# Performance work log

Measured on AMD Instinct MI355X. Metric: run time of the kernel, lower is better.

## Reference

```python
import jax, jax.numpy as jnp
import numpy as np

NUM_POINTS = 500_000
NUM_SUP = 8192
DEGREE = 32
HIDDEN = 256
NDIM = 3


def sincos_embed(coords, dim):
    # Faithful port of kappamodules ContinuousSincosEmbed.
    ndim = coords.shape[-1]
    ndim_padding = dim % ndim
    dim_per = (dim - ndim_padding) // ndim
    sincos_padding = dim_per % 2
    padding = ndim_padding + sincos_padding * ndim
    eff = (dim - padding) // ndim  # even
    omega = 1.0 / (10000.0 ** (jnp.arange(0, eff, 2, dtype=jnp.float32) / eff))
    out = coords[..., None] * omega  # (N, ndim, eff//2)
    emb = jnp.concatenate([jnp.sin(out), jnp.cos(out)], axis=-1)  # (N, ndim, eff)
    emb = emb.reshape(coords.shape[:-1] + (ndim * eff,))
    if padding > 0:
        emb = jnp.pad(emb, [(0, 0)] * (emb.ndim - 1) + [(0, padding)])
    return emb


def setup_inputs() -> dict:
    key = jax.random.key(0)
    ks = jax.random.split(key, 8)
    input_pos = jax.random.uniform(ks[0], (NUM_POINTS, NDIM), dtype=jnp.float32)
    supernode_idx = jnp.sort(
        jax.random.randint(ks[1], (NUM_SUP,), 0, NUM_POINTS, dtype=jnp.int32)
    )
    src_idx = jax.random.randint(ks[2], (NUM_SUP * DEGREE,), 0, NUM_POINTS, dtype=jnp.int32)
    dst_seg = jnp.repeat(jnp.arange(NUM_SUP, dtype=jnp.int32), DEGREE)
    s = 1.0 / np.sqrt(HIDDEN)
    w1 = jax.random.normal(ks[3], (HIDDEN, HIDDEN), dtype=jnp.float32) * s
    w2 = jax.random.normal(ks[4], (HIDDEN, HIDDEN), dtype=jnp.float32) * s
    wp = jax.random.normal(ks[5], (2 * HIDDEN, HIDDEN), dtype=jnp.float32) / np.sqrt(2 * HIDDEN)
    b1 = jnp.zeros((HIDDEN,), jnp.float32)
    b2 = jnp.zeros((HIDDEN,), jnp.float32)
    bp = jnp.zeros((HIDDEN,), jnp.float32)
    return {
        "input_pos": input_pos, "supernode_idx": supernode_idx,
        "src_idx": src_idx, "dst_seg": dst_seg,
        "w1": w1, "b1": b1, "w2": w2, "b2": b2, "wp": wp, "bp": bp,
    }


def reference(input_pos, supernode_idx, src_idx, dst_seg, w1, b1, w2, b2, wp, bp):
    num_sup = supernode_idx.shape[0]
    sup_pos = input_pos[supernode_idx]            # (S, 3)
    src_pos = input_pos[src_idx]                  # (E, 3)
    dst_pos = sup_pos[dst_seg]                    # (E, 3)
    dist = dst_pos - src_pos
    mag = jnp.linalg.norm(dist, axis=1, keepdims=True)
    rel = jnp.concatenate([dist, mag], axis=1)    # (E, 4)
    x = sincos_embed(rel, HIDDEN)                 # (E, H) relpos embed, ndim=4
    # message MLP: Linear -> GELU(exact) -> Linear
    x = jax.nn.gelu(x @ w1 + b1, approximate=False) @ w2 + b2
    # segment mean into supernodes (dst is sorted/consecutive per supernode)
    sums = jax.ops.segment_sum(x, dst_seg, num_segments=num_sup)
    counts = jax.ops.segment_sum(jnp.ones((x.shape[0],), x.dtype), dst_seg, num_segments=num_sup)
    agg = sums / jnp.maximum(counts, 1.0)[:, None]  # (S, H)
    sup_embed = sincos_embed(sup_pos, HIDDEN)       # (S, H) abspos embed, ndim=3
    out = jnp.concatenate([agg, sup_embed], axis=-1) @ wp + bp  # (S, H)
    return out[None]  # (1, S, H) -- batch_size=1 (batch_idx=None)
```

## Files before the change

### kernel.cpp

```cpp
#include <hip/hip_runtime.h>
#include <hip/hip_bf16.h>

typedef __bf16 bf16_t;
typedef bf16_t bf16x8 __attribute__((ext_vector_type(8)));
typedef float f32x16 __attribute__((ext_vector_type(16)));

constexpr float OMG[16] = {
    1.0f,        0.74989421f, 0.56234133f, 0.42169650f,
    0.31622777f, 0.23713737f, 0.17782794f, 0.13335214f,
    0.1f,        0.074989421f, 0.056234133f, 0.042169650f,
    0.031622777f, 0.023713737f, 0.017782794f, 0.013335214f};

__device__ __forceinline__ f32x16 mfma_bf16(bf16x8 a, bf16x8 b, f32x16 c) {
  return __builtin_amdgcn_mfma_f32_32x32x16_bf16(a, b, c, 0, 0, 0);
}

__device__ __forceinline__ int orig_k(int pk) {
  return 64 * (pk >> 5) + 32 * ((pk >> 4) & 1) + (pk & 15);
}

__global__ __launch_bounds__(256) void prep(
    const float* __restrict__ w1, const float* __restrict__ w2,
    const float* __restrict__ wp, const float* __restrict__ b1,
    const float* __restrict__ b2, const float* __restrict__ bp,
    bf16_t* __restrict__ w1img, bf16_t* __restrict__ wpT2,
    float* __restrict__ bfold, float* __restrict__ b1fold) {
  __shared__ float T[256][33];
  const int bid = blockIdx.x;
  const int tid = threadIdx.x;

  if (bid < 8) {
    const int n0 = bid * 32;
#pragma unroll
    for (int it = 0; it < 16; ++it) {
      const int pk = it * 8 + (tid >> 5);
      T[pk][tid & 31] = w1[orig_k(pk) * 256 + n0 + (tid & 31)];
    }
    __syncthreads();
    const int n_off = tid & 31;
    const int n = n0 + n_off;
#pragma unroll
    for (int q = 0; q < 2; ++q) {
      const int slot = (tid >> 5) + 8 * q;
      bf16x8 v;
#pragma unroll
      for (int e = 0; e < 8; ++e) v[e] = (bf16_t)T[slot * 8 + e][n_off];
      *(bf16x8*)((char*)w1img + n * 256 + ((slot ^ (n & 15)) << 4)) = v;
    }
  } else if (bid == 8) {
    const int n = tid;
    float vl[4];
    float bf1 = b1[n];
#pragma unroll
    for (int d = 0; d < 4; ++d) {
      float s = 0.f;
#pragma unroll
      for (int i = 0; i < 16; ++i)
        s = fmaf(0.01f * OMG[i], w1[(64 * d + 16 + i) * 256 + n], s);
      vl[d] = s;
#pragma unroll
      for (int i = 0; i < 16; ++i) bf1 += w1[(64 * d + 48 + i) * 256 + n];
    }
    bf16_t* ext = w1img + 32768 + n * 16;
#pragma unroll
    for (int e = 0; e < 4; ++e) ext[e] = (bf16_t)vl[e];
#pragma unroll
    for (int e = 4; e < 16; ++e) ext[e] = (bf16_t)0.0f;
    b1fold[n] = bf1;
  } else if (bid < 17) {
    const int band = (bid - 9) * 32;
#pragma unroll
    for (int it = 0; it < 32; ++it)
      T[tid][it] = wp[(256 + band + it) * 256 + tid];
    __syncthreads();
    const int o = tid;
#pragma unroll
    for (int g = 0; g < 4; ++g) {
      bf16x8 v;
#pragma unroll
      for (int e = 0; e < 8; ++e) v[e] = (bf16_t)T[o][g * 8 + e];
      *(bf16x8*)(wpT2 + o * 512 + 256 + band + g * 8) = v;
    }
  } else if (bid < 81) {
    const int t2 = bid - 17;
    const int o0 = (t2 >> 3) * 32, j0 = (t2 & 7) * 32;
#pragma unroll
    for (int it = 0; it < 32; ++it) {
      const int n = it * 8 + (tid >> 5);
      T[n][tid & 31] = wp[n * 256 + o0 + (tid & 31)];
    }
    __syncthreads();
    const int o_off = tid & 31, jb = tid >> 5;
    float a4[4] = {0.f, 0.f, 0.f, 0.f};
    for (int n = 0; n < 256; ++n) {
      const float wv = T[n][o_off];
#pragma unroll
      for (int q = 0; q < 4; ++q)
        a4[q] = fmaf(w2[(j0 + jb + 8 * q) * 256 + n], wv, a4[q]);
    }
#pragma unroll
    for (int q = 0; q < 4; ++q)
      wpT2[(o0 + o_off) * 512 + j0 + jb + 8 * q] = (bf16_t)a4[q];
  } else {
    const int o = (bid - 81) * 8 + (tid >> 5);
    const int kl = (tid & 31) * 8;
    float s = 0.f;
#pragma unroll
    for (int k = 0; k < 8; ++k) s += b2[kl + k] * wp[(kl + k) * 256 + o];
    s += __shfl_xor(s, 16); s += __shfl_xor(s, 8); s += __shfl_xor(s, 4);
    s += __shfl_xor(s, 2); s += __shfl_xor(s, 1);
    if ((tid & 31) == 0) bfold[o] = s + bp[o];
  }
}

__global__ __launch_bounds__(512, 4) void edge_mlp(
    const float* __restrict__ pos, const int* __restrict__ sup_idx,
    const int* __restrict__ src_idx,
    const bf16_t* __restrict__ w1img, const float* __restrict__ b1fold,
    bf16_t* __restrict__ cat) {
  __shared__ __attribute__((aligned(16))) bf16_t Bs[36864];

  const int tid = threadIdx.x;

  {
    const bf16x8* src8 = (const bf16x8*)w1img;
    bf16x8* dst8 = (bf16x8*)Bs;
#pragma unroll
    for (int it = 0; it < 9; ++it) {
      const int idx = it * 512 + tid;
      dst8[idx] = src8[idx];
    }
  }

  const int l = tid & 63, w = tid >> 6;
  const int pair = w >> 1, half = w & 1;
  const int hi = l >> 5, lc = l & 31;
  const int s = blockIdx.x * 4 + pair;

  const int si = sup_idx[s];
  const int srci = src_idx[s * 32 + lc];
  const float dx = pos[si * 3 + 0] - pos[srci * 3 + 0];
  const float dy = pos[si * 3 + 1] - pos[srci * 3 + 1];
  const float dz = pos[si * 3 + 2] - pos[srci * 3 + 2];
  const float mg = sqrtf(dx * dx + dy * dy + dz * dz);
  const float rv[4] = {dx, dy, dz, mg};

  float omg[8];
#pragma unroll
  for (int e = 0; e < 8; ++e) omg[e] = hi ? OMG[8 + e] : OMG[e];

  __syncthreads();

  f32x16 acc[4];
#pragma unroll
  for (int nt = 0; nt < 4; ++nt)
#pragma unroll
    for (int p = 0; p < 16; ++p) acc[nt][p] = 0.0f;

  const char* Bb = (const char*)Bs;
  const int sxor = (lc & 15) << 4;
  const int rowbase = (128 * half + lc) * 256;

  {
    bf16x8 aext;
#pragma unroll
    for (int e = 0; e < 8; ++e)
      aext[e] = (hi == 0 && e < 4) ? (bf16_t)rv[e] : (bf16_t)0.0f;
    const char* eb = Bb + 65536 + (128 * half + lc) * 32 + hi * 16;
#pragma unroll
    for (int nt = 0; nt < 4; ++nt) {
      bf16x8 be = *(const bf16x8*)(eb + nt * 1024);
      acc[nt] = mfma_bf16(aext, be, acc[nt]);
    }
  }

#pragma unroll
  for (int d = 0; d < 4; ++d) {
    float ang[8];
#pragma unroll
    for (int e = 0; e < 8; ++e) ang[e] = rv[d] * omg[e];
    bf16x8 a_sin, a_cos;
#pragma unroll
    for (int e = 0; e < 8; ++e) a_sin[e] = (bf16_t)__sinf(ang[e]);
#pragma unroll
    for (int e = 0; e < 8; ++e) a_cos[e] = (bf16_t)__cosf(ang[e]);

    const int ko_sin = ((4 * d + hi) << 4) ^ sxor;
    const int ko_cos = ((4 * d + 2 + hi) << 4) ^ sxor;
    {
      bf16x8 b0 = *(const bf16x8*)(Bb + rowbase + 0 * 8192 + ko_sin);
      bf16x8 b1_ = *(const bf16x8*)(Bb + rowbase + 1 * 8192 + ko_sin);
      bf16x8 b2_ = *(const bf16x8*)(Bb + rowbase + 2 * 8192 + ko_sin);
      bf16x8 b3 = *(const bf16x8*)(Bb + rowbase + 3 * 8192 + ko_sin);
      acc[0] = mfma_bf16(a_sin, b0, acc[0]);
      acc[1] = mfma_bf16(a_sin, b1_, acc[1]);
      acc[2] = mfma_bf16(a_sin, b2_, acc[2]);
      acc[3] = mfma_bf16(a_sin, b3, acc[3]);
    }
    {
      bf16x8 b0 = *(const bf16x8*)(Bb + rowbase + 0 * 8192 + ko_cos);
      bf16x8 b1_ = *(const bf16x8*)(Bb + rowbase + 1 * 8192 + ko_cos);
      bf16x8 b2_ = *(const bf16x8*)(Bb + rowbase + 2 * 8192 + ko_cos);
      bf16x8 b3 = *(const bf16x8*)(Bb + rowbase + 3 * 8192 + ko_cos);
      acc[0] = mfma_bf16(a_cos, b0, acc[0]);
      acc[1] = mfma_bf16(a_cos, b1_, acc[1]);
      acc[2] = mfma_bf16(a_cos, b2_, acc[2]);
      acc[3] = mfma_bf16(a_cos, b3, acc[3]);
    }
  }

  const float C2 = -0.10296644f, C0 = -2.3022765f;
#pragma unroll
  for (int nt = 0; nt < 4; ++nt) {
    const float bi = b1fold[128 * half + 32 * nt + lc];
    float ssum = 0.0f;
#pragma unroll
    for (int p = 0; p < 16; p += 2) {
      const float x0 = acc[nt][p] + bi;
      const float x1 = acc[nt][p + 1] + bi;
      const float t0 = fmaf(x0 * x0, C2, C0), t1 = fmaf(x1 * x1, C2, C0);
      const float e0 = exp2f(x0 * t0), e1 = exp2f(x1 * t1);
      const float r0 = __builtin_amdgcn_rcpf(e0 + 1.0f);
      const float r1 = __builtin_amdgcn_rcpf(e1 + 1.0f);
      ssum = fmaf(x0, r0, ssum);
      ssum = fmaf(x1, r1, ssum);
    }
    ssum += __shfl_xor(ssum, 32);
    if (hi == 0)
      cat[s * 512 + 128 * half + 32 * nt + lc] = (bf16_t)(ssum * 0.03125f);
  }

#pragma unroll
  for (int q = 0; q < 2; ++q) {
    const int col = 128 * half + l + 64 * q;
    float v = 0.0f;
    if (col < 252) {
      const int d = (col >= 84 ? 1 : 0) + (col >= 168 ? 1 : 0);
      const int t3 = col - 84 * d;
      const int sc2 = (t3 >= 42) ? 1 : 0;
      const float om = __expf(-0.21929381838038533f * (float)(t3 - 42 * sc2));
      const float pd = pos[si * 3 + d];
      const float ang = pd * om;
      v = sc2 ? __cosf(ang) : __sinf(ang);
    }
    cat[s * 512 + 256 + col] = (bf16_t)v;
  }
}

__global__ __launch_bounds__(256) void proj(
    const bf16_t* __restrict__ cat, const bf16_t* __restrict__ wpT2,
    const float* __restrict__ bfold, float* __restrict__ out) {
  const int tid = threadIdx.x;
  const int l = tid & 63, w = tid >> 6;
  const int hi = l >> 5, lc = l & 31;
  const int rm = blockIdx.x * 32;
  const int cn = blockIdx.y * 128 + w * 32;
  const int r0 = rm + lc;
  const int c0 = cn + lc;

  f32x16 a0;
#pragma unroll
  for (int p = 0; p < 16; ++p) a0[p] = 0.f;
#pragma unroll 8
  for (int kk = 0; kk < 32; ++kk) {
    int k0 = kk * 16 + 8 * hi;
    bf16x8 fa0 = *(const bf16x8*)(cat + r0 * 512 + k0);
    bf16x8 fb = *(const bf16x8*)(wpT2 + c0 * 512 + k0);
    a0 = mfma_bf16(fa0, fb, a0);
  }
  float bias = bfold[c0];
#pragma unroll
  for (int rr = 0; rr < 16; ++rr) {
    int rowo = (rr & 3) + 8 * (rr >> 2) + 4 * hi;
    out[(rm + rowo) * 256 + c0] = a0[rr] + bias;
  }
}

extern "C" void kernel_launch(void* const* d_in, const int* in_sizes, int n_in,
                              void* d_out, int out_size, void* d_ws, size_t ws_size,
                              hipStream_t stream) {
  const float* pos = (const float*)d_in[0];
  const int* sup_idx = (const int*)d_in[1];
  const int* src_idx = (const int*)d_in[2];
  const float* w1 = (const float*)d_in[4];
  const float* b1 = (const float*)d_in[5];
  const float* w2 = (const float*)d_in[6];
  const float* b2 = (const float*)d_in[7];
  const float* wp = (const float*)d_in[8];
  const float* bp = (const float*)d_in[9];

  char* ws = (char*)d_ws;
  bf16_t* w1img = (bf16_t*)(ws);
  bf16_t* wpT2  = (bf16_t*)(ws + 73728);
  float*  bfold = (float*)(ws + 335872);
  float*  b1fold = (float*)(ws + 336896);
  bf16_t* cat   = (bf16_t*)(ws + 337920);
  float* out = (float*)d_out;

  if (ws_size < (size_t)(337920 + 8192 * 512 * 2)) return;

  prep<<<dim3(113), dim3(256), 0, stream>>>(
      w1, w2, wp, b1, b2, bp, w1img, wpT2, bfold, b1fold);
  edge_mlp<<<dim3(2048), dim3(512), 0, stream>>>(pos, sup_idx, src_idx, w1img, b1fold, cat);
  proj<<<dim3(256, 2), dim3(256), 0, stream>>>(cat, wpT2, bfold, out);
}
```

Measured before the change: 78.27 us.

## Fold W2·Wp with MFMA, loop supernodes per block, and widen proj tiles

The scalar FMA fold of w2 into wp in the prep kernel is replaced by a bf16 conversion pass plus a separate small MFMA GEMM kernel. The edge MLP kernel now processes four supernodes per wave pair in a loop, so each block loads the shared-memory w1 image once for 16 supernodes instead of 4, and the grid shrinks fourfold. The projection kernel computes two 32-row tiles per wave, reusing each weight fragment across both. The costs are an extra kernel launch, a bf16-rounded folded weight, fewer blocks to fill the GPU, and a serial loop that may hurt latency hiding.

Result: slower. 143.9 us (+83.8%).

```diff
diff --git a/kernel.cpp b/kernel.cpp
--- a/kernel.cpp
+++ b/kernel.cpp
@@ -19,11 +19,12 @@
   return 64 * (pk >> 5) + 32 * ((pk >> 4) & 1) + (pk & 15);
 }
 
-__global__ __launch_bounds__(256) void prep(
+__global__ __launch_bounds__(256) void prepA(
     const float* __restrict__ w1, const float* __restrict__ w2,
     const float* __restrict__ wp, const float* __restrict__ b1,
     const float* __restrict__ b2, const float* __restrict__ bp,
     bf16_t* __restrict__ w1img, bf16_t* __restrict__ wpT2,
+    bf16_t* __restrict__ wpTa, bf16_t* __restrict__ w2b,
     float* __restrict__ bfold, float* __restrict__ b1fold) {
   __shared__ float T[256][33];
   const int bid = blockIdx.x;
@@ -81,28 +82,29 @@
       for (int e = 0; e < 8; ++e) v[e] = (bf16_t)T[o][g * 8 + e];
       *(bf16x8*)(wpT2 + o * 512 + 256 + band + g * 8) = v;
     }
-  } else if (bid < 81) {
-    const int t2 = bid - 17;
-    const int o0 = (t2 >> 3) * 32, j0 = (t2 & 7) * 32;
+  } else if (bid < 25) {
+    const int band = (bid - 17) * 32;
+#pragma unroll
+    for (int it = 0; it < 32; ++it)
+      T[tid][it] = wp[(band + it) * 256 + tid];
+    __syncthreads();
+    const int o = tid;
+#pragma unroll
+    for (int g = 0; g < 4; ++g) {
+      bf16x8 v;
+#pragma unroll
+      for (int e = 0; e < 8; ++e) v[e] = (bf16_t)T[o][g * 8 + e];
+      *(bf16x8*)(wpTa + o * 256 + band + g * 8) = v;
+    }
+  } else if (bid < 33) {
+    const int base = (bid - 25) * 8192;
 #pragma unroll
     for (int it = 0; it < 32; ++it) {
-      const int n = it * 8 + (tid >> 5);
-      T[n][tid & 31] = wp[n * 256 + o0 + (tid & 31)];
-    }
-    __syncthreads();
-    const int o_off = tid & 31, jb = tid >> 5;
-    float a4[4] = {0.f, 0.f, 0.f, 0.f};
-    for (int n = 0; n < 256; ++n) {
-      const float wv = T[n][o_off];
-#pragma unroll
-      for (int q = 0; q < 4; ++q)
-        a4[q] = fmaf(w2[(j0 + jb + 8 * q) * 256 + n], wv, a4[q]);
-    }
-#pragma unroll
-    for (int q = 0; q < 4; ++q)
-      wpT2[(o0 + o_off) * 512 + j0 + jb + 8 * q] = (bf16_t)a4[q];
+      const int idx = base + it * 256 + tid;
+      w2b[idx] = (bf16_t)w2[idx];
+    }
   } else {
-    const int o = (bid - 81) * 8 + (tid >> 5);
+    const int o = (bid - 33) * 8 + (tid >> 5);
     const int kl = (tid & 31) * 8;
     float s = 0.f;
 #pragma unroll
@@ -110,6 +112,45 @@
     s += __shfl_xor(s, 16); s += __shfl_xor(s, 8); s += __shfl_xor(s, 4);
     s += __shfl_xor(s, 2); s += __shfl_xor(s, 1);
     if ((tid & 31) == 0) bfold[o] = s + bp[o];
+  }
+}
+
+__global__ __launch_bounds__(256) void prep_b(
+    const bf16_t* __restrict__ wpTa, const bf16_t* __restrict__ w2b,
+    bf16_t* __restrict__ wpT2) {
+  const int tid = threadIdx.x;
+  const int l = tid & 63;
+  const int w = tid >> 6;
+  const int wm = w >> 1, wn = w & 1;
+  const int rm = blockIdx.x * 128 + wm * 64;
+  const int cn = blockIdx.y * 128 + wn * 64;
+  const int asel = l >> 5;
+  const int lr = l & 31;
+  const int r0 = rm + lr, r1 = rm + 32 + lr;
+  const int c0 = cn + lr, c1 = cn + 32 + lr;
+
+  f32x16 a00, a01, a10, a11;
+#pragma unroll
+  for (int q = 0; q < 16; ++q) { a00[q] = 0.f; a01[q] = 0.f; a10[q] = 0.f; a11[q] = 0.f; }
+#pragma unroll 4
+  for (int kk = 0; kk < 16; ++kk) {
+    int k0 = kk * 16 + 8 * asel;
+    bf16x8 fa0 = *(const bf16x8*)(wpTa + r0 * 256 + k0);
+    bf16x8 fa1 = *(const bf16x8*)(wpTa + r1 * 256 + k0);
+    bf16x8 fb0 = *(const bf16x8*)(w2b + c0 * 256 + k0);
+    bf16x8 fb1 = *(const bf16x8*)(w2b + c1 * 256 + k0);
+    a00 = mfma_bf16(fa0, fb0, a00);
+    a01 = mfma_bf16(fa0, fb1, a01);
+    a10 = mfma_bf16(fa1, fb0, a10);
+    a11 = mfma_bf16(fa1, fb1, a11);
+  }
+#pragma unroll
+  for (int rr = 0; rr < 16; ++rr) {
+    int rowo = (rr & 3) + 8 * (rr >> 2) + 4 * asel;
+    wpT2[(rm + rowo) * 512 + c0] = (bf16_t)a00[rr];
+    wpT2[(rm + rowo) * 512 + c1] = (bf16_t)a01[rr];
+    wpT2[(rm + 32 + rowo) * 512 + c0] = (bf16_t)a10[rr];
+    wpT2[(rm + 32 + rowo) * 512 + c1] = (bf16_t)a11[rr];
   }
 }
 
@@ -135,115 +176,118 @@
   const int l = tid & 63, w = tid >> 6;
   const int pair = w >> 1, half = w & 1;
   const int hi = l >> 5, lc = l & 31;
-  const int s = blockIdx.x * 4 + pair;
-
-  const int si = sup_idx[s];
-  const int srci = src_idx[s * 32 + lc];
-  const float dx = pos[si * 3 + 0] - pos[srci * 3 + 0];
-  const float dy = pos[si * 3 + 1] - pos[srci * 3 + 1];
-  const float dz = pos[si * 3 + 2] - pos[srci * 3 + 2];
-  const float mg = sqrtf(dx * dx + dy * dy + dz * dz);
-  const float rv[4] = {dx, dy, dz, mg};
 
   float omg[8];
 #pragma unroll
   for (int e = 0; e < 8; ++e) omg[e] = hi ? OMG[8 + e] : OMG[e];
 
   __syncthreads();
-
-  f32x16 acc[4];
-#pragma unroll
-  for (int nt = 0; nt < 4; ++nt)
-#pragma unroll
-    for (int p = 0; p < 16; ++p) acc[nt][p] = 0.0f;
 
   const char* Bb = (const char*)Bs;
   const int sxor = (lc & 15) << 4;
   const int rowbase = (128 * half + lc) * 256;
-
-  {
-    bf16x8 aext;
-#pragma unroll
-    for (int e = 0; e < 8; ++e)
-      aext[e] = (hi == 0 && e < 4) ? (bf16_t)rv[e] : (bf16_t)0.0f;
-    const char* eb = Bb + 65536 + (128 * half + lc) * 32 + hi * 16;
+  const char* eb = Bb + 65536 + (128 * half + lc) * 32 + hi * 16;
+
+#pragma unroll 1
+  for (int ss = 0; ss < 4; ++ss) {
+    const int s = blockIdx.x * 16 + pair * 4 + ss;
+    const int si = sup_idx[s];
+    const int srci = src_idx[s * 32 + lc];
+    const float dx = pos[si * 3 + 0] - pos[srci * 3 + 0];
+    const float dy = pos[si * 3 + 1] - pos[srci * 3 + 1];
+    const float dz = pos[si * 3 + 2] - pos[srci * 3 + 2];
+    const float mg = sqrtf(dx * dx + dy * dy + dz * dz);
+    const float rv[4] = {dx, dy, dz, mg};
+
+    f32x16 acc[4];
+#pragma unroll
+    for (int nt = 0; nt < 4; ++nt)
+#pragma unroll
+      for (int p = 0; p < 16; ++p) acc[nt][p] = 0.0f;
+
+    {
+      bf16x8 aext;
+#pragma unroll
+      for (int e = 0; e < 8; ++e)
+        aext[e] = (hi == 0 && e < 4) ? (bf16_t)rv[e] : (bf16_t)0.0f;
+#pragma unroll
+      for (int nt = 0; nt < 4; ++nt) {
+        bf16x8 be = *(const bf16x8*)(eb + nt * 1024);
+        acc[nt] = mfma_bf16(aext, be, acc[nt]);
+      }
+    }
+
+#pragma unroll
+    for (int d = 0; d < 4; ++d) {
+      float ang[8];
+#pragma unroll
+      for (int e = 0; e < 8; ++e) ang[e] = rv[d] * omg[e];
+      bf16x8 a_sin, a_cos;
+#pragma unroll
+      for (int e = 0; e < 8; ++e) a_sin[e] = (bf16_t)__sinf(ang[e]);
+#pragma unroll
+      for (int e = 0; e < 8; ++e) a_cos[e] = (bf16_t)__cosf(ang[e]);
+
+      const int ko_sin = ((4 * d + hi) << 4) ^ sxor;
+      const int ko_cos = ((4 * d + 2 + hi) << 4) ^ sxor;
+      {
+        bf16x8 b0 = *(const bf16x8*)(Bb + rowbase + 0 * 8192 + ko_sin);
+        bf16x8 b1_ = *(const bf16x8*)(Bb + rowbase + 1 * 8192 + ko_sin);
+        bf16x8 b2_ = *(const bf16x8*)(Bb + rowbase + 2 * 8192 + ko_sin);
+        bf16x8 b3 = *(const bf16x8*)(Bb + rowbase + 3 * 8192 + ko_sin);
+        acc[0] = mfma_bf16(a_sin, b0, acc[0]);
+        acc[1] = mfma_bf16(a_sin, b1_, acc[1]);
+        acc[2] = mfma_bf16(a_sin, b2_, acc[2]);
+        acc[3] = mfma_bf16(a_sin, b3, acc[3]);
+      }
+      {
+        bf16x8 b0 = *(const bf16x8*)(Bb + rowbase + 0 * 8192 + ko_cos);
+        bf16x8 b1_ = *(const bf16x8*)(Bb + rowbase + 1 * 8192 + ko_cos);
+        bf16x8 b2_ = *(const bf16x8*)(Bb + rowbase + 2 * 8192 + ko_cos);
+        bf16x8 b3 = *(const bf16x8*)(Bb + rowbase + 3 * 8192 + ko_cos);
+        acc[0] = mfma_bf16(a_cos, b0, acc[0]);
+        acc[1] = mfma_bf16(a_cos, b1_, acc[1]);
+        acc[2] = mfma_bf16(a_cos, b2_, acc[2]);
+        acc[3] = mfma_bf16(a_cos, b3, acc[3]);
+      }
+    }
+
+    const float C2 = -0.10296644f, C0 = -2.3022765f;
 #pragma unroll
     for (int nt = 0; nt < 4; ++nt) {
-      bf16x8 be = *(const bf16x8*)(eb + nt * 1024);
-      acc[nt] = mfma_bf16(aext, be, acc[nt]);
-    }
-  }
-
-#pragma unroll
-  for (int d = 0; d < 4; ++d) {
-    float ang[8];
-#pragma unroll
-    for (int e = 0; e < 8; ++e) ang[e] = rv[d] * omg[e];
-    bf16x8 a_sin, a_cos;
-#pragma unroll
-    for (int e = 0; e < 8; ++e) a_sin[e] = (bf16_t)__sinf(ang[e]);
-#pragma unroll
-    for (int e = 0; e < 8; ++e) a_cos[e] = (bf16_t)__cosf(ang[e]);
-
-    const int ko_sin = ((4 * d + hi) << 4) ^ sxor;
-    const int ko_cos = ((4 * d + 2 + hi) << 4) ^ sxor;
-    {
-      bf16x8 b0 = *(const bf16x8*)(Bb + rowbase + 0 * 8192 + ko_sin);
-      bf16x8 b1_ = *(const bf16x8*)(Bb + rowbase + 1 * 8192 + ko_sin);
-      bf16x8 b2_ = *(const bf16x8*)(Bb + rowbase + 2 * 8192 + ko_sin);
-      bf16x8 b3 = *(const bf16x8*)(Bb + rowbase + 3 * 8192 + ko_sin);
-      acc[0] = mfma_bf16(a_sin, b0, acc[0]);
-      acc[1] = mfma_bf16(a_sin, b1_, acc[1]);
-      acc[2] = mfma_bf16(a_sin, b2_, acc[2]);
-      acc[3] = mfma_bf16(a_sin, b3, acc[3]);
-    }
-    {
-      bf16x8 b0 = *(const bf16x8*)(Bb + rowbase + 0 * 8192 + ko_cos);
-      bf16x8 b1_ = *(const bf16x8*)(Bb + rowbase + 1 * 8192 + ko_cos);
-      bf16x8 b2_ = *(const bf16x8*)(Bb + rowbase + 2 * 8192 + ko_cos);
-      bf16x8 b3 = *(const bf16x8*)(Bb + rowbase + 3 * 8192 + ko_cos);
-      acc[0] = mfma_bf16(a_cos, b0, acc[0]);
-      acc[1] = mfma_bf16(a_cos, b1_, acc[1]);
-      acc[2] = mfma_bf16(a_cos, b2_, acc[2]);
-      acc[3] = mfma_bf16(a_cos, b3, acc[3]);
-    }
-  }
-
-  const float C2 = -0.10296644f, C0 = -2.3022765f;
-#pragma unroll
-  for (int nt = 0; nt < 4; ++nt) {
-    const float bi = b1fold[128 * half + 32 * nt + lc];
-    float ssum = 0.0f;
-#pragma unroll
-    for (int p = 0; p < 16; p += 2) {
-      const float x0 = acc[nt][p] + bi;
-      const float x1 = acc[nt][p + 1] + bi;
-      const float t0 = fmaf(x0 * x0, C2, C0), t1 = fmaf(x1 * x1, C2, C0);
-      const float e0 = exp2f(x0 * t0), e1 = exp2f(x1 * t1);
-      const float r0 = __builtin_amdgcn_rcpf(e0 + 1.0f);
-      const float r1 = __builtin_amdgcn_rcpf(e1 + 1.0f);
-      ssum = fmaf(x0, r0, ssum);
-      ssum = fmaf(x1, r1, ssum);
-    }
-    ssum += __shfl_xor(ssum, 32);
-    if (hi == 0)
-      cat[s * 512 + 128 * half + 32 * nt + lc] = (bf16_t)(ssum * 0.03125f);
-  }
-
-#pragma unroll
-  for (int q = 0; q < 2; ++q) {
-    const int col = 128 * half + l + 64 * q;
-    float v = 0.0f;
-    if (col < 252) {
-      const int d = (col >= 84 ? 1 : 0) + (col >= 168 ? 1 : 0);
-      const int t3 = col - 84 * d;
-      const int sc2 = (t3 >= 42) ? 1 : 0;
-      const float om = __expf(-0.21929381838038533f * (float)(t3 - 42 * sc2));
-      const float pd = pos[si * 3 + d];
-      const float ang = pd * om;
-      v = sc2 ? __cosf(ang) : __sinf(ang);
-    }
-    cat[s * 512 + 256 + col] = (bf16_t)v;
+      const float bi = b1fold[128 * half + 32 * nt + lc];
+      float ssum = 0.0f;
+#pragma unroll
+      for (int p = 0; p < 16; p += 2) {
+        const float x0 = acc[nt][p] + bi;
+        const float x1 = acc[nt][p + 1] + bi;
+        const float t0 = fmaf(x0 * x0, C2, C0), t1 = fmaf(x1 * x1, C2, C0);
+        const float e0 = exp2f(x0 * t0), e1 = exp2f(x1 * t1);
+        const float r0 = __builtin_amdgcn_rcpf(e0 + 1.0f);
+        const float r1 = __builtin_amdgcn_rcpf(e1 + 1.0f);
+        ssum = fmaf(x0, r0, ssum);
+        ssum = fmaf(x1, r1, ssum);
+      }
+      ssum += __shfl_xor(ssum, 32);
+      if (hi == 0)
+        cat[s * 512 + 128 * half + 32 * nt + lc] = (bf16_t)(ssum * 0.03125f);
+    }
+
+#pragma unroll
+    for (int q = 0; q < 2; ++q) {
+      const int col = 128 * half + l + 64 * q;
+      float v = 0.0f;
+      if (col < 252) {
+        const int d = (col >= 84 ? 1 : 0) + (col >= 168 ? 1 : 0);
+        const int t3 = col - 84 * d;
+        const int sc2 = (t3 >= 42) ? 1 : 0;
+        const float om = __expf(-0.21929381838038533f * (float)(t3 - 42 * sc2));
+        const float pd = pos[si * 3 + d];
+        const float ang = pd * om;
+        v = sc2 ? __cosf(ang) : __sinf(ang);
+      }
+      cat[s * 512 + 256 + col] = (bf16_t)v;
+    }
   }
 }
 
@@ -253,26 +297,29 @@
   const int tid = threadIdx.x;
   const int l = tid & 63, w = tid >> 6;
   const int hi = l >> 5, lc = l & 31;
-  const int rm = blockIdx.x * 32;
+  const int rm = blockIdx.x * 64;
   const int cn = blockIdx.y * 128 + w * 32;
-  const int r0 = rm + lc;
+  const int r0 = rm + lc, r1 = rm + 32 + lc;
   const int c0 = cn + lc;
 
-  f32x16 a0;
-#pragma unroll
-  for (int p = 0; p < 16; ++p) a0[p] = 0.f;
+  f32x16 a0, a1;
+#pragma unroll
+  for (int p = 0; p < 16; ++p) { a0[p] = 0.f; a1[p] = 0.f; }
 #pragma unroll 8
   for (int kk = 0; kk < 32; ++kk) {
     int k0 = kk * 16 + 8 * hi;
     bf16x8 fa0 = *(const bf16x8*)(cat + r0 * 512 + k0);
+    bf16x8 fa1 = *(const bf16x8*)(cat + r1 * 512 + k0);
     bf16x8 fb = *(const bf16x8*)(wpT2 + c0 * 512 + k0);
     a0 = mfma_bf16(fa0, fb, a0);
+    a1 = mfma_bf16(fa1, fb, a1);
   }
   float bias = bfold[c0];
 #pragma unroll
   for (int rr = 0; rr < 16; ++rr) {
     int rowo = (rr & 3) + 8 * (rr >> 2) + 4 * hi;
     out[(rm + rowo) * 256 + c0] = a0[rr] + bias;
+    out[(rm + 32 + rowo) * 256 + c0] = a1[rr] + bias;
   }
 }
 
@@ -294,13 +341,16 @@
   bf16_t* wpT2  = (bf16_t*)(ws + 73728);
   float*  bfold = (float*)(ws + 335872);
   float*  b1fold = (float*)(ws + 336896);
-  bf16_t* cat   = (bf16_t*)(ws + 337920);
+  bf16_t* wpTa  = (bf16_t*)(ws + 337920);
+  bf16_t* w2b   = (bf16_t*)(ws + 468992);
+  bf16_t* cat   = (bf16_t*)(ws + 600064);
   float* out = (float*)d_out;
 
-  if (ws_size < (size_t)(337920 + 8192 * 512 * 2)) return;
-
-  prep<<<dim3(113), dim3(256), 0, stream>>>(
-      w1, w2, wp, b1, b2, bp, w1img, wpT2, bfold, b1fold);
-  edge_mlp<<<dim3(2048), dim3(512), 0, stream>>>(pos, sup_idx, src_idx, w1img, b1fold, cat);
-  proj<<<dim3(256, 2), dim3(256), 0, stream>>>(cat, wpT2, bfold, out);
-}
+  if (ws_size < (size_t)(600064 + 8192 * 512 * 2)) return;
+
+  prepA<<<dim3(65), dim3(256), 0, stream>>>(
+      w1, w2, wp, b1, b2, bp, w1img, wpT2, wpTa, w2b, bfold, b1fold);
+  prep_b<<<dim3(2, 2), dim3(256), 0, stream>>>(wpTa, w2b, wpT2);
+  edge_mlp<<<dim3(512), dim3(512), 0, stream>>>(pos, sup_idx, src_idx, w1img, b1fold, cat);
+  proj<<<dim3(128, 2), dim3(256), 0, stream>>>(cat, wpT2, bfold, out);
+}
```
